# Performance work log

Hardware: AMD Instinct MI355X
Metric: run time of the kernel (lower is better)

## Reference

```python
import jax, jax.numpy as jnp
import numpy as np

B, S, D = 2, 2048, 1024
H, HD = 16, 64  # num_heads, hidden_size per head


def setup_inputs() -> dict:
    key = jax.random.key(0)
    ks = jax.random.split(key, 10)
    inp = {
        'queries': jax.random.normal(ks[0], (B, S, D), jnp.float32),
        'keys': jax.random.normal(ks[1], (B, S, D), jnp.float32),
        'values': jax.random.normal(ks[2], (B, S, D), jnp.float32),
        # binary indicator masks (some zeros so renorm guard path is exercised)
        'ind_q': (jax.random.uniform(ks[3], (B, S)) > 0.2).astype(jnp.float32),
        'ind_k': (jax.random.uniform(ks[4], (B, S)) > 0.2).astype(jnp.float32),
        'ind_v': (jax.random.uniform(ks[5], (B, S)) > 0.2).astype(jnp.float32),
        'Wq': jax.random.normal(ks[6], (D, H * HD), jnp.float32) / np.sqrt(D),
        'Wk': jax.random.normal(ks[7], (D, H * HD), jnp.float32) / np.sqrt(D),
        'Wv': jax.random.normal(ks[8], (D, H * HD), jnp.float32) / np.sqrt(D),
        'Wo': jax.random.normal(ks[9], (H * HD, D), jnp.float32) / np.sqrt(H * HD),
    }
    return inp


def reference(queries, keys, values, ind_q, ind_k, ind_v, Wq, Wk, Wv, Wo):
    b, nq, _ = queries.shape
    nk = keys.shape[1]
    # projections -> [B, H, S, HD], masked by indicators
    Q = (queries @ Wq).reshape(b, nq, H, HD).transpose(0, 2, 1, 3) * ind_q[:, None, :, None]
    K = (keys @ Wk).reshape(b, nk, H, HD).transpose(0, 2, 1, 3) * ind_k[:, None, :, None]
    V = (values @ Wv).reshape(b, nk, H, HD).transpose(0, 2, 1, 3) * ind_v[:, None, :, None]
    # scaled dot-product scores, plain softmax over keys
    scores = jnp.einsum('bhqd,bhkd->bhqk', Q, K) / jnp.sqrt(jnp.float32(HD))
    attn = jax.nn.softmax(scores, axis=-1)
    # post-softmax multiplicative key-indicator mask + renormalization with zero-row guard
    attn = attn * ind_k[:, None, None, :]
    denom = jnp.sum(attn, axis=-1, keepdims=True)
    attn = attn / jnp.where(denom == 0.0, 1.0, denom)
    out = jnp.einsum('bhqk,bhkd->bhqd', attn, V)  # [B, H, Q, HD]
    out = out.transpose(0, 2, 1, 3).reshape(b, nq, H * HD)
    return out @ Wo
```

## Files before the change

### kernel.cpp

```cpp
#include <hip/hip_runtime.h>
#include <math.h>

typedef __attribute__((ext_vector_type(8))) short bf16x8;
typedef __attribute__((ext_vector_type(4))) float f32x4;

__device__ __forceinline__ unsigned short f2b(float f) {
    union { float f; unsigned int u; } v; v.f = f;
    unsigned int u = v.u + 0x7FFFu + ((v.u >> 16) & 1u);
    return (unsigned short)(u >> 16);
}

__device__ __forceinline__ f32x4 mfma16(bf16x8 a, bf16x8 b, f32x4 c) {
    return __builtin_amdgcn_mfma_f32_16x16x32_bf16(a, b, c, 0, 0, 0);
}

__device__ __forceinline__ void async_ld16(void* l, const void* g) {
    __builtin_amdgcn_global_load_lds(
        (__attribute__((address_space(1))) void*)g,
        (__attribute__((address_space(3))) void*)l, 16, 0, 0);
}

__device__ __forceinline__ float exp2_hw(float x) {
    float r; asm("v_exp_f32 %0, %1" : "=v"(r) : "v"(x)); return r;
}

__device__ __forceinline__ unsigned int cvtpk_bf16(float a, float b) {
    unsigned int r;
    asm("v_cvt_pk_bf16_f32 %0, %1, %2" : "=v"(r) : "v"(a), "v"(b));
    return r;
}

__global__ __launch_bounds__(256) void cvt3(
    const float* __restrict__ q, const float* __restrict__ k,
    const float* __restrict__ v, unsigned short* __restrict__ qo,
    unsigned short* __restrict__ ko, unsigned short* __restrict__ vo)
{
    const int z = blockIdx.z;
    const float* in = (z == 0) ? q : (z == 1) ? k : v;
    unsigned short* out = (z == 0) ? qo : (z == 1) ? ko : vo;
    const int i = (blockIdx.x * 256 + threadIdx.x) * 4;
    const float4 x = *(const float4*)(in + i);
    ushort4 o; o.x = f2b(x.x); o.y = f2b(x.y); o.z = f2b(x.z); o.w = f2b(x.w);
    *(ushort4*)(out + i) = o;
}

__global__ __launch_bounds__(256) void cvt_tr(
    const float* __restrict__ W0, const float* __restrict__ W1,
    const float* __restrict__ W2, const float* __restrict__ W3,
    unsigned short* __restrict__ T0, unsigned short* __restrict__ T1,
    unsigned short* __restrict__ T2, unsigned short* __restrict__ T3)
{
    const int z = blockIdx.z;
    const float* W = (z == 0) ? W0 : (z == 1) ? W1 : (z == 2) ? W2 : W3;
    unsigned short* T = (z == 0) ? T0 : (z == 1) ? T1 : (z == 2) ? T2 : T3;
    __shared__ short Ls[64 * 65];
    const int t = threadIdx.x;
    const int k0 = blockIdx.x * 64, n0 = blockIdx.y * 64;
#pragma unroll
    for (int ii = 0; ii < 4; ++ii) {
        const int kl = (t >> 4) + 16 * ii, nl = (t & 15) * 4;
        const float4 v = *(const float4*)&W[(size_t)(k0 + kl) * 1024 + n0 + nl];
        Ls[kl * 65 + nl + 0] = (short)f2b(v.x);
        Ls[kl * 65 + nl + 1] = (short)f2b(v.y);
        Ls[kl * 65 + nl + 2] = (short)f2b(v.z);
        Ls[kl * 65 + nl + 3] = (short)f2b(v.w);
    }
    __syncthreads();
#pragma unroll
    for (int ii = 0; ii < 4; ++ii) {
        const int nl = (t >> 4) + 16 * ii, kl = (t & 15) * 4;
        ushort4 o;
        o.x = (unsigned short)Ls[(kl + 0) * 65 + nl];
        o.y = (unsigned short)Ls[(kl + 1) * 65 + nl];
        o.z = (unsigned short)Ls[(kl + 2) * 65 + nl];
        o.w = (unsigned short)Ls[(kl + 3) * 65 + nl];
        *(ushort4*)&T[(size_t)(n0 + nl) * 1024 + k0 + kl] = o;
    }
}

__global__ __launch_bounds__(256) void gemm_proj3(
    const unsigned short* __restrict__ qb, const unsigned short* __restrict__ kb,
    const unsigned short* __restrict__ vb,
    const unsigned short* __restrict__ Wqt, const unsigned short* __restrict__ Wkt,
    const unsigned short* __restrict__ Wvt,
    unsigned short* __restrict__ Qw, unsigned short* __restrict__ Kw,
    unsigned short* __restrict__ Vw,
    const float* __restrict__ iq, const float* __restrict__ ik,
    const float* __restrict__ iv)
{
    const int z = blockIdx.z;
    const unsigned short* A  = (z == 0) ? qb  : (z == 1) ? kb  : vb;
    const unsigned short* Bt = (z == 0) ? Wqt : (z == 1) ? Wkt : Wvt;
    unsigned short* Cw       = (z == 0) ? Qw  : (z == 1) ? Kw  : Vw;
    const float* msk         = (z == 0) ? iq  : (z == 1) ? ik  : iv;
    const float scale = (z == 0) ? 0.125f * 1.44269504088896f : 1.0f;

    __shared__ __align__(16) short As[128 * 32];
    __shared__ __align__(16) short Bs[128 * 32];
    __shared__ float maskL[128];
    const int t = threadIdx.x;
    const int w = t >> 6, lane = t & 63, l15 = lane & 15, quad = lane >> 4;
    const int wr = w >> 1, wc = w & 1;
    const int n0 = blockIdx.x * 128, m0 = blockIdx.y * 128;
    if (t < 128) maskL[t] = msk[m0 + t] * scale;

    const int srow = lane >> 2, soff = (lane & 3) * 8;

    f32x4 zero4 = {0.f, 0.f, 0.f, 0.f};
    f32x4 acc[4][4];
#pragma unroll
    for (int i = 0; i < 4; ++i)
#pragma unroll
        for (int j = 0; j < 4; ++j) acc[i][j] = zero4;

    for (int k0 = 0; k0 < 1024; k0 += 32) {
        __syncthreads();
#pragma unroll
        for (int i = 0; i < 2; ++i) {
            const int r = 16 * (2 * w + i);
            async_ld16(As + r * 32, A + (size_t)(m0 + r + srow) * 1024 + k0 + soff);
            async_ld16(Bs + r * 32, Bt + (size_t)(n0 + r + srow) * 1024 + k0 + soff);
        }
        __syncthreads();
        bf16x8 af[4], bfr[4];
#pragma unroll
        for (int i = 0; i < 4; ++i)
            af[i] = *(const bf16x8*)&As[(64 * wr + 16 * i + l15) * 32 + 8 * quad];
#pragma unroll
        for (int j = 0; j < 4; ++j)
            bfr[j] = *(const bf16x8*)&Bs[(64 * wc + 16 * j + l15) * 32 + 8 * quad];
#pragma unroll
        for (int i = 0; i < 4; ++i)
#pragma unroll
            for (int j = 0; j < 4; ++j)
                acc[i][j] = mfma16(af[i], bfr[j], acc[i][j]);
    }

    const int h = 2 * blockIdx.x + wc;
#pragma unroll
    for (int i = 0; i < 4; ++i)
#pragma unroll
        for (int j = 0; j < 4; ++j)
#pragma unroll
            for (int reg = 0; reg < 4; ++reg) {
                const int mloc = 64 * wr + 16 * i + 4 * quad + reg;
                const int m = m0 + mloc;
                const int bb = m >> 11, s = m & 2047;
                const int hd = 16 * j + l15;
                Cw[((size_t)(bb * 16 + h) * 2048 + s) * 64 + hd] =
                    f2b(acc[i][j][reg] * maskL[mloc]);
            }
}

__global__ __launch_bounds__(256) void gemm_out(
    const unsigned short* __restrict__ A, const unsigned short* __restrict__ Bt,
    float* __restrict__ C)
{
    __shared__ __align__(16) short As[128 * 32];
    __shared__ __align__(16) short Bs[64 * 32];
    const int t = threadIdx.x;
    const int w = t >> 6, lane = t & 63, l15 = lane & 15, quad = lane >> 4;
    const int wr = w >> 1, wc = w & 1;
    const int n0 = blockIdx.x * 64, m0 = blockIdx.y * 128;
    const int srow = lane >> 2, soff = (lane & 3) * 8;

    f32x4 zero4 = {0.f, 0.f, 0.f, 0.f};
    f32x4 acc[4][2];
#pragma unroll
    for (int i = 0; i < 4; ++i) { acc[i][0] = zero4; acc[i][1] = zero4; }

    for (int k0 = 0; k0 < 1024; k0 += 32) {
        __syncthreads();
#pragma unroll
        for (int i = 0; i < 2; ++i) {
            const int r = 16 * (2 * w + i);
            async_ld16(As + r * 32, A + (size_t)(m0 + r + srow) * 1024 + k0 + soff);
        }
        async_ld16(Bs + (16 * w) * 32, Bt + (size_t)(n0 + 16 * w + srow) * 1024 + k0 + soff);
        __syncthreads();
        bf16x8 af[4], bfr[2];
#pragma unroll
        for (int i = 0; i < 4; ++i)
            af[i] = *(const bf16x8*)&As[(64 * wr + 16 * i + l15) * 32 + 8 * quad];
#pragma unroll
        for (int j = 0; j < 2; ++j)
            bfr[j] = *(const bf16x8*)&Bs[(32 * wc + 16 * j + l15) * 32 + 8 * quad];
#pragma unroll
        for (int i = 0; i < 4; ++i)
#pragma unroll
            for (int j = 0; j < 2; ++j)
                acc[i][j] = mfma16(af[i], bfr[j], acc[i][j]);
    }
#pragma unroll
    for (int i = 0; i < 4; ++i)
#pragma unroll
        for (int j = 0; j < 2; ++j)
#pragma unroll
            for (int reg = 0; reg < 4; ++reg) {
                const int m = m0 + 64 * wr + 16 * i + 4 * quad + reg;
                const int n = n0 + 32 * wc + 16 * j + l15;
                C[(size_t)m * 1024 + n] = acc[i][j][reg];
            }
}

#define GST 72

__global__ __launch_bounds__(256, 4) void attn_mfma(
    const unsigned short* __restrict__ Qw, const unsigned short* __restrict__ Kw,
    const unsigned short* __restrict__ Vw, const float* __restrict__ indk,
    unsigned short* __restrict__ AO)
{
    __shared__ __align__(16) short Ks[2][64 * GST];
    __shared__ __align__(16) short Vt[2][64 * GST];
    __shared__ float biask[2][64];
    const int t = threadIdx.x;
    const int w = t >> 6, lane = t & 63, l15 = lane & 15, quad = lane >> 4;
    const unsigned wg = (blockIdx.x & 7) * 128 + (blockIdx.x >> 3);
    const int q0 = (wg & 31) * 64;
    const int h = (wg >> 5) & 15, b = wg >> 9;
    const size_t base = (size_t)(b * 16 + h) * (2048 * 64);
    const unsigned short* Qb = Qw + base + (size_t)q0 * 64;
    const unsigned short* Kb = Kw + base;
    const unsigned short* Vb = Vw + base;

    bf16x8 qf[2];
    qf[0] = *(const bf16x8*)&Qb[(16 * w + l15) * 64 + 8 * quad];
    qf[1] = *(const bf16x8*)&Qb[(16 * w + l15) * 64 + 32 + 8 * quad];

    ushort4 kreg[4], vreg[4];
    float breg = 0.f;
#pragma unroll
    for (int u = 0; u < 4; ++u)
        kreg[u] = *(const ushort4*)&Kb[(size_t)((t >> 4) + 16 * u) * 64 + (t & 15) * 4];
#pragma unroll
    for (int u = 0; u < 2; ++u) {
        const int idx = t + 256 * u;
        const int dq = idx >> 5, kp2 = (idx & 31) * 2;
        vreg[2 * u]     = *(const ushort4*)&Vb[(size_t)kp2 * 64 + 4 * dq];
        vreg[2 * u + 1] = *(const ushort4*)&Vb[(size_t)(kp2 + 1) * 64 + 4 * dq];
    }
    if (t < 64) breg = indk[b * 2048 + t];

    const int u_ = l15 >> 2, a_ = l15 & 3;
    const int krA = 8 * u_ + 4 * (u_ & 1) + a_;
    const int krB = 8 * u_ + 4 * (1 - (u_ & 1)) + a_;

    f32x4 zero4 = {0.f, 0.f, 0.f, 0.f};
    f32x4 oacc[4];
    oacc[0] = zero4; oacc[1] = zero4; oacc[2] = zero4; oacc[3] = zero4;
    float l_part = 0.f;

    for (int c = 0; c < 32; ++c) {
        const int cur = c & 1;
#pragma unroll
        for (int u = 0; u < 4; ++u) {
            const int krow = (t >> 4) + 16 * u;
            const int lrow = krow ^ (((krow >> 3) & 1) << 2);
            *(ushort4*)&Ks[cur][lrow * GST + (t & 15) * 4] = kreg[u];
        }
#pragma unroll
        for (int u = 0; u < 2; ++u) {
            const int idx = t + 256 * u;
            const int dq = idx >> 5, kp2 = (idx & 31) * 2;
            const unsigned int* v0d = (const unsigned int*)&vreg[2 * u];
            const unsigned int* v1d = (const unsigned int*)&vreg[2 * u + 1];
            *(unsigned int*)&Vt[cur][(4 * dq + 0) * GST + kp2] =
                __builtin_amdgcn_perm(v1d[0], v0d[0], 0x05040100u);
            *(unsigned int*)&Vt[cur][(4 * dq + 1) * GST + kp2] =
                __builtin_amdgcn_perm(v1d[0], v0d[0], 0x07060302u);
            *(unsigned int*)&Vt[cur][(4 * dq + 2) * GST + kp2] =
                __builtin_amdgcn_perm(v1d[1], v0d[1], 0x05040100u);
            *(unsigned int*)&Vt[cur][(4 * dq + 3) * GST + kp2] =
                __builtin_amdgcn_perm(v1d[1], v0d[1], 0x07060302u);
        }
        if (t < 64) biask[cur][t] = (breg - 1.f) * 1e30f;
        __syncthreads();
        {
            const int kn = (c < 31 ? c + 1 : 31) * 64;
#pragma unroll
            for (int u = 0; u < 4; ++u)
                kreg[u] = *(const ushort4*)&Kb[(size_t)(kn + (t >> 4) + 16 * u) * 64 + (t & 15) * 4];
#pragma unroll
            for (int u = 0; u < 2; ++u) {
                const int idx = t + 256 * u;
                const int dq = idx >> 5, kp2 = (idx & 31) * 2;
                vreg[2 * u]     = *(const ushort4*)&Vb[(size_t)(kn + kp2) * 64 + 4 * dq];
                vreg[2 * u + 1] = *(const ushort4*)&Vb[(size_t)(kn + kp2 + 1) * 64 + 4 * dq];
            }
            if (t < 64) breg = indk[b * 2048 + kn + t];
        }
        const short* KsC = Ks[cur];
        const short* VtC = Vt[cur];

        f32x4 sacc[4];
#pragma unroll
        for (int g = 0; g < 4; ++g) {
            const float4 bv = *(const float4*)&biask[cur][32 * (g >> 1) + 4 * (g & 1) + 8 * quad];
            sacc[g][0] = bv.x; sacc[g][1] = bv.y; sacc[g][2] = bv.z; sacc[g][3] = bv.w;
        }
        __builtin_amdgcn_s_setprio(1);
#pragma unroll
        for (int ks = 0; ks < 2; ++ks)
#pragma unroll
            for (int g = 0; g < 4; ++g) {
                const int row = 32 * (g >> 1) + ((g & 1) ? krB : krA);
                const bf16x8 kf = *(const bf16x8*)&KsC[row * GST + 32 * ks + 8 * quad];
                sacc[g] = mfma16(kf, qf[ks], sacc[g]);
            }
        __builtin_amdgcn_s_setprio(0);

        unsigned int dw[4][2];
#pragma unroll
        for (int g = 0; g < 4; ++g) {
#pragma unroll
            for (int r = 0; r < 4; ++r) sacc[g][r] = exp2_hw(sacc[g][r]);
            dw[g][0] = cvtpk_bf16(sacc[g][0], sacc[g][1]);
            dw[g][1] = cvtpk_bf16(sacc[g][2], sacc[g][3]);
        }

        __builtin_amdgcn_s_setprio(1);
#pragma unroll
        for (int ks = 0; ks < 2; ++ks) {
            union { unsigned int u[4]; bf16x8 b; } pc;
            pc.u[0] = dw[2 * ks][0];     pc.u[1] = dw[2 * ks][1];
            pc.u[2] = dw[2 * ks + 1][0]; pc.u[3] = dw[2 * ks + 1][1];
#pragma unroll
            for (int nj = 0; nj < 4; ++nj) {
                const bf16x8 vbf = *(const bf16x8*)
                    &VtC[(16 * nj + l15) * GST + 32 * ks + 8 * quad];
                oacc[nj] = mfma16(pc.b, vbf, oacc[nj]);
            }
        }
        __builtin_amdgcn_s_setprio(0);

        float rg[4];
#pragma unroll
        for (int g = 0; g < 4; ++g)
            rg[g] = (sacc[g][0] + sacc[g][1]) + (sacc[g][2] + sacc[g][3]);
        l_part += (rg[0] + rg[1]) + (rg[2] + rg[3]);
    }

    float l = l_part;
    l += __shfl_xor(l, 16);
    l += __shfl_xor(l, 32);
    const float inv = (l > 0.f) ? 1.f / l : 0.f;
    float invr[4];
#pragma unroll
    for (int r = 0; r < 4; ++r) invr[r] = __shfl(inv, 4 * quad + r);
#pragma unroll
    for (int nj = 0; nj < 4; ++nj)
#pragma unroll
        for (int r = 0; r < 4; ++r) {
            const int row = q0 + 16 * w + 4 * quad + r;
            AO[(size_t)(b * 2048 + row) * 1024 + h * 64 + 16 * nj + l15] =
                f2b(oacc[nj][r] * invr[r]);
        }
}

extern "C" void kernel_launch(void* const* d_in, const int* in_sizes, int n_in,
                              void* d_out, int out_size, void* d_ws, size_t ws_size,
                              hipStream_t stream) {
    const float* q  = (const float*)d_in[0];
    const float* k  = (const float*)d_in[1];
    const float* v  = (const float*)d_in[2];
    const float* iq = (const float*)d_in[3];
    const float* ik = (const float*)d_in[4];
    const float* iv = (const float*)d_in[5];
    const float* Wq = (const float*)d_in[6];
    const float* Wk = (const float*)d_in[7];
    const float* Wv = (const float*)d_in[8];
    const float* Wo = (const float*)d_in[9];
    float* out = (float*)d_out;
    unsigned short* ws = (unsigned short*)d_ws;

    const size_t M1 = 1048576;
    unsigned short* qb  = ws;
    unsigned short* kb  = ws + 4  * M1;
    unsigned short* vb  = ws + 8  * M1;
    unsigned short* Wqt = ws + 12 * M1;
    unsigned short* Wkt = ws + 13 * M1;
    unsigned short* Wvt = ws + 14 * M1;
    unsigned short* Wot = ws + 15 * M1;
    unsigned short* Qw  = ws + 16 * M1;
    unsigned short* Kw  = ws + 20 * M1;
    unsigned short* Vw  = ws + 24 * M1;
    unsigned short* AO  = ws + 28 * M1;

    cvt3<<<dim3(4096, 1, 3), dim3(256), 0, stream>>>(q, k, v, qb, kb, vb);
    cvt_tr<<<dim3(16, 16, 4), dim3(256), 0, stream>>>(Wq, Wk, Wv, Wo, Wqt, Wkt, Wvt, Wot);
    gemm_proj3<<<dim3(8, 32, 3), dim3(256), 0, stream>>>(
        qb, kb, vb, Wqt, Wkt, Wvt, Qw, Kw, Vw, iq, ik, iv);
    attn_mfma<<<dim3(1024, 1, 1), dim3(256), 0, stream>>>(Qw, Kw, Vw, ik, AO);
    gemm_out<<<dim3(16, 32), dim3(256), 0, stream>>>(AO, Wot, out);
}
```

Before: 259.7 us.

## Double attention query tile to 128 rows per 512-thread block, preload key bias

Each attention workgroup now has 8 waves covering 128 query rows, so every K/V tile staged in LDS serves twice as many queries and the grid halves. Each thread loads a smaller slice of K and V per iteration. The key-indicator bias for all 2048 keys is precomputed once into LDS instead of being reloaded every chunk. In exchange, LDS use per block grows by 8KB and occupancy per CU may change with the 512-thread launch bounds.

```diff
diff --git a/kernel.cpp b/kernel.cpp
--- a/kernel.cpp
+++ b/kernel.cpp
@@ -205,19 +205,19 @@
 
 #define GST 72
 
-__global__ __launch_bounds__(256, 4) void attn_mfma(
+__global__ __launch_bounds__(512, 4) void attn_mfma(
     const unsigned short* __restrict__ Qw, const unsigned short* __restrict__ Kw,
     const unsigned short* __restrict__ Vw, const float* __restrict__ indk,
     unsigned short* __restrict__ AO)
 {
     __shared__ __align__(16) short Ks[2][64 * GST];
     __shared__ __align__(16) short Vt[2][64 * GST];
-    __shared__ float biask[2][64];
+    __shared__ float Bl[2048];
     const int t = threadIdx.x;
     const int w = t >> 6, lane = t & 63, l15 = lane & 15, quad = lane >> 4;
-    const unsigned wg = (blockIdx.x & 7) * 128 + (blockIdx.x >> 3);
-    const int q0 = (wg & 31) * 64;
-    const int h = (wg >> 5) & 15, b = wg >> 9;
+    const unsigned wg = (blockIdx.x & 7) * 64 + (blockIdx.x >> 3);
+    const int q0 = (wg & 15) * 128;
+    const int h = (wg >> 4) & 15, b = wg >> 8;
     const size_t base = (size_t)(b * 16 + h) * (2048 * 64);
     const unsigned short* Qb = Qw + base + (size_t)q0 * 64;
     const unsigned short* Kb = Kw + base;
@@ -227,19 +227,23 @@
     qf[0] = *(const bf16x8*)&Qb[(16 * w + l15) * 64 + 8 * quad];
     qf[1] = *(const bf16x8*)&Qb[(16 * w + l15) * 64 + 32 + 8 * quad];
 
-    ushort4 kreg[4], vreg[4];
-    float breg = 0.f;
-#pragma unroll
-    for (int u = 0; u < 4; ++u)
-        kreg[u] = *(const ushort4*)&Kb[(size_t)((t >> 4) + 16 * u) * 64 + (t & 15) * 4];
-#pragma unroll
-    for (int u = 0; u < 2; ++u) {
-        const int idx = t + 256 * u;
-        const int dq = idx >> 5, kp2 = (idx & 31) * 2;
-        vreg[2 * u]     = *(const ushort4*)&Vb[(size_t)kp2 * 64 + 4 * dq];
-        vreg[2 * u + 1] = *(const ushort4*)&Vb[(size_t)(kp2 + 1) * 64 + 4 * dq];
-    }
-    if (t < 64) breg = indk[b * 2048 + t];
+    {
+        const float4 bi = *(const float4*)&indk[b * 2048 + t * 4];
+        float4 bo;
+        bo.x = (bi.x - 1.f) * 1e30f; bo.y = (bi.y - 1.f) * 1e30f;
+        bo.z = (bi.z - 1.f) * 1e30f; bo.w = (bi.w - 1.f) * 1e30f;
+        *(float4*)&Bl[t * 4] = bo;
+    }
+
+    const int skr = t >> 3, skc = (t & 7) * 8;
+    const int slr = skr ^ (((skr >> 3) & 1) << 2);
+    const int dq = t >> 5, kp2 = (t & 31) * 2;
+
+    bf16x8 kreg;
+    ushort4 vreg[2];
+    kreg = *(const bf16x8*)&Kb[(size_t)skr * 64 + skc];
+    vreg[0] = *(const ushort4*)&Vb[(size_t)kp2 * 64 + 4 * dq];
+    vreg[1] = *(const ushort4*)&Vb[(size_t)(kp2 + 1) * 64 + 4 * dq];
 
     const int u_ = l15 >> 2, a_ = l15 & 3;
     const int krA = 8 * u_ + 4 * (u_ & 1) + a_;
@@ -252,18 +256,10 @@
 
     for (int c = 0; c < 32; ++c) {
         const int cur = c & 1;
-#pragma unroll
-        for (int u = 0; u < 4; ++u) {
-            const int krow = (t >> 4) + 16 * u;
-            const int lrow = krow ^ (((krow >> 3) & 1) << 2);
-            *(ushort4*)&Ks[cur][lrow * GST + (t & 15) * 4] = kreg[u];
-        }
-#pragma unroll
-        for (int u = 0; u < 2; ++u) {
-            const int idx = t + 256 * u;
-            const int dq = idx >> 5, kp2 = (idx & 31) * 2;
-            const unsigned int* v0d = (const unsigned int*)&vreg[2 * u];
-            const unsigned int* v1d = (const unsigned int*)&vreg[2 * u + 1];
+        *(bf16x8*)&Ks[cur][slr * GST + skc] = kreg;
+        {
+            const unsigned int* v0d = (const unsigned int*)&vreg[0];
+            const unsigned int* v1d = (const unsigned int*)&vreg[1];
             *(unsigned int*)&Vt[cur][(4 * dq + 0) * GST + kp2] =
                 __builtin_amdgcn_perm(v1d[0], v0d[0], 0x05040100u);
             *(unsigned int*)&Vt[cur][(4 * dq + 1) * GST + kp2] =
@@ -273,29 +269,21 @@
             *(unsigned int*)&Vt[cur][(4 * dq + 3) * GST + kp2] =
                 __builtin_amdgcn_perm(v1d[1], v0d[1], 0x07060302u);
         }
-        if (t < 64) biask[cur][t] = (breg - 1.f) * 1e30f;
         __syncthreads();
         {
             const int kn = (c < 31 ? c + 1 : 31) * 64;
-#pragma unroll
-            for (int u = 0; u < 4; ++u)
-                kreg[u] = *(const ushort4*)&Kb[(size_t)(kn + (t >> 4) + 16 * u) * 64 + (t & 15) * 4];
-#pragma unroll
-            for (int u = 0; u < 2; ++u) {
-                const int idx = t + 256 * u;
-                const int dq = idx >> 5, kp2 = (idx & 31) * 2;
-                vreg[2 * u]     = *(const ushort4*)&Vb[(size_t)(kn + kp2) * 64 + 4 * dq];
-                vreg[2 * u + 1] = *(const ushort4*)&Vb[(size_t)(kn + kp2 + 1) * 64 + 4 * dq];
-            }
-            if (t < 64) breg = indk[b * 2048 + kn + t];
+            kreg = *(const bf16x8*)&Kb[(size_t)(kn + skr) * 64 + skc];
+            vreg[0] = *(const ushort4*)&Vb[(size_t)(kn + kp2) * 64 + 4 * dq];
+            vreg[1] = *(const ushort4*)&Vb[(size_t)(kn + kp2 + 1) * 64 + 4 * dq];
         }
         const short* KsC = Ks[cur];
         const short* VtC = Vt[cur];
+        const float* BlC = Bl + c * 64;
 
         f32x4 sacc[4];
 #pragma unroll
         for (int g = 0; g < 4; ++g) {
-            const float4 bv = *(const float4*)&biask[cur][32 * (g >> 1) + 4 * (g & 1) + 8 * quad];
+            const float4 bv = *(const float4*)&BlC[32 * (g >> 1) + 4 * (g & 1) + 8 * quad];
             sacc[g][0] = bv.x; sacc[g][1] = bv.y; sacc[g][2] = bv.z; sacc[g][3] = bv.w;
         }
         __builtin_amdgcn_s_setprio(1);
@@ -390,6 +378,6 @@
     cvt_tr<<<dim3(16, 16, 4), dim3(256), 0, stream>>>(Wq, Wk, Wv, Wo, Wqt, Wkt, Wvt, Wot);
     gemm_proj3<<<dim3(8, 32, 3), dim3(256), 0, stream>>>(
         qb, kb, vb, Wqt, Wkt, Wvt, Qw, Kw, Vw, iq, ik, iv);
-    attn_mfma<<<dim3(1024, 1, 1), dim3(256), 0, stream>>>(Qw, Kw, Vw, ik, AO);
+    attn_mfma<<<dim3(512, 1, 1), dim3(512), 0, stream>>>(Qw, Kw, Vw, ik, AO);
     gemm_out<<<dim3(16, 32), dim3(256), 0, stream>>>(AO, Wot, out);
 }
```

Measured after the change: 227.4 us. 12.4% less time.
